# Performance work log

Hardware: AMD Instinct MI355X
Metric: run time of the kernel (lower is better)

Reference implementation:

```python
import jax, jax.numpy as jnp
import numpy as np

NUM_HEADS = 16
HIDDEN = 1024
DIM = HIDDEN // NUM_HEADS  # 64
NEG = -1e8
LN_EPS = 1e-5


def setup_inputs() -> dict:
    key = jax.random.key(0)
    ks = jax.random.split(key, 8)
    B, Lq, Lk = 8, 512, 2048
    s = 0.02
    return {
        "input_embed": jax.random.normal(ks[0], (B, Lq, HIDDEN), jnp.float32),
        "kg_embed": jax.random.normal(ks[1], (B, Lk, HIDDEN), jnp.float32),
        "input_mask": jnp.ones((B, Lq), jnp.float32),
        "kg_mask": jnp.ones((B, Lk), jnp.float32),
        "Wq": jax.random.normal(ks[2], (DIM, DIM), jnp.float32) * s,
        "Wk": jax.random.normal(ks[3], (DIM, DIM), jnp.float32) * s,
        "Wv": jax.random.normal(ks[4], (DIM, DIM), jnp.float32) * s,
        "W_lin": jax.random.normal(ks[5], (HIDDEN, HIDDEN), jnp.float32) * s,
        "b_lin": jnp.zeros((HIDDEN,), jnp.float32),
        "ln_gamma": jnp.ones((HIDDEN,), jnp.float32),
        "ln_beta": jnp.zeros((HIDDEN,), jnp.float32),
    }


def reference(input_embed, kg_embed, input_mask, kg_mask, Wq, Wk, Wv, W_lin, b_lin, ln_gamma, ln_beta):
    B, Lq, H = input_embed.shape
    Lk = kg_embed.shape[1]
    # split heads: per-head slices share the SAME dim x dim q/k/v weights
    xq = input_embed.reshape(B, Lq, NUM_HEADS, DIM)
    xk = kg_embed.reshape(B, Lk, NUM_HEADS, DIM)
    q = jnp.einsum('bqhd,ed->bqhe', xq, Wq)  # Linear: x @ W.T
    k = jnp.einsum('bkhd,ed->bkhe', xk, Wk)
    v = jnp.einsum('bkhd,ed->bkhe', xk, Wv)
    scores = jnp.einsum('bqhd,bkhd->bhqk', q, k) / np.sqrt(DIM)  # [B,H,Lq,Lk]
    # additive masks: query-side and key-side
    scores = scores + ((1.0 - input_mask) * NEG)[:, None, :, None] \
                    + ((1.0 - kg_mask) * NEG)[:, None, None, :]
    attn = jax.nn.softmax(scores, axis=-1)
    ctx = jnp.einsum('bhqk,bkhd->bqhd', attn, v).reshape(B, Lq, H)  # concat heads
    lin = ctx @ W_lin.T + b_lin
    x = jax.nn.gelu(lin, approximate=False) + input_embed  # nn.GELU() is exact erf
    mu = jnp.mean(x, axis=-1, keepdims=True)
    var = jnp.mean(jnp.square(x - mu), axis=-1, keepdims=True)
    return (x - mu) * jax.lax.rsqrt(var + LN_EPS) * ln_gamma + ln_beta
```

## Files before the change

### kernel.cpp

```cpp
#include <hip/hip_runtime.h>
#include <cstdint>

#define BATCH 8
#define LQ 512
#define LK 2048
#define NH 16
#define DIM 64
#define HID 1024
#define NTOK (BATCH * LQ)
#define NKT (LK / 64)
#define SC 0.1803368801111204f
#define NEGM (-1.4426950408889634e8f)

typedef _Float16 f16x8 __attribute__((ext_vector_type(8)));
typedef __fp16 half2v __attribute__((ext_vector_type(2)));
typedef float f32x4 __attribute__((ext_vector_type(4)));

#define MFMA(a, b, c) __builtin_amdgcn_mfma_f32_16x16x32_f16((a), (b), (c), 0, 0, 0)

__device__ __forceinline__ f16x8 ld8(const _Float16* p) { return *(const f16x8*)p; }

__device__ __forceinline__ void gl_lds16(const void* g, void* l) {
  __builtin_amdgcn_global_load_lds(
      (const __attribute__((address_space(1))) uint32_t*)g,
      (__attribute__((address_space(3))) uint32_t*)l, 16, 0, 0);
}

__device__ __forceinline__ f16x8 cvt8(const float* p) {
  const float4 a = *(const float4*)p;
  const float4 b = *(const float4*)(p + 4);
  f16x8 v;
  v[0] = (_Float16)a.x; v[1] = (_Float16)a.y; v[2] = (_Float16)a.z; v[3] = (_Float16)a.w;
  v[4] = (_Float16)b.x; v[5] = (_Float16)b.y; v[6] = (_Float16)b.z; v[7] = (_Float16)b.w;
  return v;
}

__device__ __forceinline__ uint2 pk4(float a, float b, float c, float d) {
  union { half2v h2[2]; uint2 u; } t;
  t.h2[0] = __builtin_amdgcn_cvt_pkrtz(a, b);
  t.h2[1] = __builtin_amdgcn_cvt_pkrtz(c, d);
  return t.u;
}

__device__ __forceinline__ f16x8 pk8(float4 a, float4 b) {
  union { half2v h2[4]; f16x8 v; } t;
  t.h2[0] = __builtin_amdgcn_cvt_pkrtz(a.x, a.y);
  t.h2[1] = __builtin_amdgcn_cvt_pkrtz(a.z, a.w);
  t.h2[2] = __builtin_amdgcn_cvt_pkrtz(b.x, b.y);
  t.h2[3] = __builtin_amdgcn_cvt_pkrtz(b.z, b.w);
  return t.v;
}

__global__ __launch_bounds__(256, 2) void attn_kernel(
    const float* __restrict__ Xq, const float* __restrict__ Xk,
    const float* __restrict__ Wq, const float* __restrict__ Wk,
    const float* __restrict__ Wv, const float* __restrict__ kg_mask,
    _Float16* __restrict__ ctx) {
  __shared__ __align__(16) float    Xl[2][64 * 64];
  __shared__ __align__(16) _Float16 Kl[64 * 72];
  __shared__ __align__(16) _Float16 Vl[64 * 72];
  __shared__ __align__(16) _Float16 Pl[4][16 * 72];
  const int tid = threadIdx.x;
  const int wave = tid >> 6, lane = tid & 63, l16 = lane & 15, quad = lane >> 4;
  const int b = blockIdx.x >> 4, h = blockIdx.x & 15;
  const int qbase = blockIdx.y * 128;
  const float* Xg = Xk + (size_t)b * LK * HID + h * 64;
  const float* mg = kg_mask + (size_t)b * LK;

  auto stageX = [&](int kt, int nbuf) {
#pragma unroll
    for (int i = 0; i < 4; ++i) {
      const int row = i * 16 + wave * 4 + (lane >> 4);
      const int c = (lane & 15) ^ (row & 7);
      gl_lds16(Xg + (size_t)(kt + row) * HID + c * 4,
               &Xl[nbuf][(i * 16 + wave * 4) * 64]);
    }
  };
  stageX(0, 0);

  f16x8 aq0[2], aq1[2];
  {
    f16x8 wq0[4], wq1[4];
#pragma unroll
    for (int nt = 0; nt < 4; ++nt) {
      const float* wp = Wq + (nt * 16 + l16) * DIM + quad * 8;
      wq0[nt] = cvt8(wp);
      wq1[nt] = cvt8(wp + 32);
    }
#pragma unroll
    for (int qt = 0; qt < 2; ++qt) {
      const int qg = qbase + qt * 64 + wave * 16 + l16;
      const float* xpq = Xq + (size_t)(b * LQ + qg) * HID + h * 64 + quad * 8;
      const f16x8 bq0 = cvt8(xpq), bq1 = cvt8(xpq + 32);
#pragma unroll
      for (int nt = 0; nt < 4; ++nt) {
        f32x4 d = {0.f, 0.f, 0.f, 0.f};
        d = MFMA(wq0[nt], bq0, d);
        d = MFMA(wq1[nt], bq1, d);
        *(uint2*)&Pl[wave][l16 * 72 + nt * 16 + quad * 4] =
            pk4(d[0] * SC, d[1] * SC, d[2] * SC, d[3] * SC);
      }
      aq0[qt] = ld8(&Pl[wave][l16 * 72 + quad * 8]);
      aq1[qt] = ld8(&Pl[wave][l16 * 72 + 32 + quad * 8]);
    }
  }

  f16x8 ak0[4], ak1[4], bv0[4], bv1[4];
#pragma unroll
  for (int nt = 0; nt < 4; ++nt) {
    const float* wp = Wk + (nt * 16 + l16) * DIM + quad * 8;
    ak0[nt] = cvt8(wp);
    ak1[nt] = cvt8(wp + 32);
    const float* vp = Wv + (nt * 16 + l16) * DIM + quad * 8;
    bv0[nt] = cvt8(vp);
    bv1[nt] = cvt8(vp + 32);
  }

  const f32x4 z4 = {0.f, 0.f, 0.f, 0.f};
  f32x4 o[2][4];
  float l_run[2] = {0.f, 0.f};
#pragma unroll
  for (int qt = 0; qt < 2; ++qt)
#pragma unroll
    for (int i = 0; i < 4; ++i) o[qt][i] = z4;

  for (int t = 0; t < NKT; ++t) {
    const int buf = t & 1;
    const int kt = t * 64;
    __syncthreads();

    const int rr = wave * 16 + l16;
    const float* xrow = &Xl[buf][rr * 64];
    const int sw8 = l16 & 7;
    const float4 c0 = *(const float4*)(xrow + (((2 * quad) ^ sw8) * 4));
    const float4 c1 = *(const float4*)(xrow + (((2 * quad + 1) ^ sw8) * 4));
    const float4 c2 = *(const float4*)(xrow + (((2 * quad + 8) ^ sw8) * 4));
    const float4 c3 = *(const float4*)(xrow + (((2 * quad + 9) ^ sw8) * 4));
    const f16x8 bx0 = pk8(c0, c1), bx1 = pk8(c2, c3);

#pragma unroll
    for (int nt = 0; nt < 4; ++nt) {
      f32x4 d = z4;
      d = MFMA(ak0[nt], bx0, d);
      d = MFMA(ak1[nt], bx1, d);
      *(uint2*)&Kl[(wave * 16 + l16) * 72 + nt * 16 + quad * 4] =
          pk4(d[0], d[1], d[2], d[3]);
    }
#pragma unroll
    for (int dt = 0; dt < 4; ++dt) {
      f32x4 d = z4;
      d = MFMA(bx0, bv0[dt], d);
      d = MFMA(bx1, bv1[dt], d);
      *(uint2*)&Vl[(dt * 16 + l16) * 72 + wave * 16 + quad * 4] =
          pk4(d[0], d[1], d[2], d[3]);
    }
    __syncthreads();

    float4 mv[4];
#pragma unroll
    for (int nt = 0; nt < 4; ++nt) {
      const float4 m4 = *(const float4*)(mg + kt + nt * 16 + quad * 4);
      mv[nt].x = (1.f - m4.x) * NEGM;
      mv[nt].y = (1.f - m4.y) * NEGM;
      mv[nt].z = (1.f - m4.z) * NEGM;
      mv[nt].w = (1.f - m4.w) * NEGM;
    }
    if (t + 1 < NKT) stageX(kt + 64, buf ^ 1);

    float p[2][4][4];
#pragma unroll
    for (int nt = 0; nt < 4; ++nt) {
      const f16x8 kb0 = ld8(&Kl[(nt * 16 + l16) * 72 + quad * 8]);
      const f16x8 kb1 = ld8(&Kl[(nt * 16 + l16) * 72 + 32 + quad * 8]);
#pragma unroll
      for (int qt = 0; qt < 2; ++qt) {
        f32x4 s = z4;
        s = MFMA(kb0, aq0[qt], s);
        s = MFMA(kb1, aq1[qt], s);
        const float e0 = __builtin_amdgcn_exp2f(s[0] + mv[nt].x);
        const float e1 = __builtin_amdgcn_exp2f(s[1] + mv[nt].y);
        const float e2 = __builtin_amdgcn_exp2f(s[2] + mv[nt].z);
        const float e3 = __builtin_amdgcn_exp2f(s[3] + mv[nt].w);
        l_run[qt] += (e0 + e1) + (e2 + e3);
        p[qt][nt][0] = e0; p[qt][nt][1] = e1; p[qt][nt][2] = e2; p[qt][nt][3] = e3;
      }
    }
    f16x8 ap0[2], ap1[2];
#pragma unroll
    for (int qt = 0; qt < 2; ++qt) {
#pragma unroll
      for (int nt = 0; nt < 4; ++nt)
        *(uint2*)&Pl[wave][l16 * 72 + nt * 16 + quad * 4] =
            pk4(p[qt][nt][0], p[qt][nt][1], p[qt][nt][2], p[qt][nt][3]);
      ap0[qt] = ld8(&Pl[wave][l16 * 72 + quad * 8]);
      ap1[qt] = ld8(&Pl[wave][l16 * 72 + 32 + quad * 8]);
    }
#pragma unroll
    for (int dt = 0; dt < 4; ++dt) {
      const f16x8 vb0 = ld8(&Vl[(dt * 16 + l16) * 72 + quad * 8]);
      const f16x8 vb1 = ld8(&Vl[(dt * 16 + l16) * 72 + 32 + quad * 8]);
#pragma unroll
      for (int qt = 0; qt < 2; ++qt) {
        o[qt][dt] = MFMA(vb0, ap0[qt], o[qt][dt]);
        o[qt][dt] = MFMA(vb1, ap1[qt], o[qt][dt]);
      }
    }
  }

  float inv[2];
#pragma unroll
  for (int qt = 0; qt < 2; ++qt) {
    float s = l_run[qt];
    s += __shfl_xor(s, 16);
    s += __shfl_xor(s, 32);
    inv[qt] = 1.f / s;
  }
#pragma unroll
  for (int qt = 0; qt < 2; ++qt) {
    const int qg = qbase + qt * 64 + wave * 16 + l16;
    _Float16* base = ctx + (size_t)(b * LQ + qg) * HID + h * 64;
#pragma unroll
    for (int dt = 0; dt < 4; ++dt)
      *(uint2*)(base + dt * 16 + quad * 4) =
          pk4(o[qt][dt][0] * inv[qt], o[qt][dt][1] * inv[qt],
              o[qt][dt][2] * inv[qt], o[qt][dt][3] * inv[qt]);
  }
}

__global__ __launch_bounds__(256) void wconv_kernel(const float* __restrict__ W,
                                                    _Float16* __restrict__ Wh) {
  const int i = blockIdx.x * 256 + threadIdx.x;
  const float4 v = ((const float4*)W)[i];
  ((uint2*)Wh)[i] = pk4(v.x, v.y, v.z, v.w);
}

__global__ __launch_bounds__(512) void linear_kernel(const _Float16* __restrict__ A,
                                                     const _Float16* __restrict__ Wh,
                                                     const float* __restrict__ bias,
                                                     const float* __restrict__ resid,
                                                     float* __restrict__ Xout) {
  __shared__ __align__(16) _Float16 Al[2][128 * 64];
  __shared__ __align__(16) _Float16 Bl[2][128 * 64];
  const int tid = threadIdx.x;
  const int wave = tid >> 6, lane = tid & 63, l16 = lane & 15, quad = lane >> 4;
  const int wm = wave >> 2, wn = wave & 3;
  const int nbase = blockIdx.x * 128, mbase = blockIdx.y * 128;
  const int srow = wave * 16 + (lane >> 3);
  const int sc = lane & 7;

  auto stage = [&](int kk, int nbuf) {
#pragma unroll
    for (int i = 0; i < 2; ++i) {
      const int row = srow + i * 8;
      const int c = sc ^ (row & 7);
      gl_lds16(A + (size_t)(mbase + row) * HID + kk + c * 8,
               &Al[nbuf][(wave * 16 + i * 8) * 64]);
      gl_lds16(Wh + (size_t)(nbase + row) * HID + kk + c * 8,
               &Bl[nbuf][(wave * 16 + i * 8) * 64]);
    }
  };

  const f32x4 z4 = {0.f, 0.f, 0.f, 0.f};
  f32x4 acc[4][2];
#pragma unroll
  for (int mt = 0; mt < 4; ++mt)
#pragma unroll
    for (int nt = 0; nt < 2; ++nt) acc[mt][nt] = z4;

  stage(0, 0);
  for (int t = 0; t < HID / 64; ++t) {
    const int buf = t & 1;
    __syncthreads();
    if (t + 1 < HID / 64) stage((t + 1) * 64, buf ^ 1);
    const int sw = l16 & 7;
    f16x8 b0[2], b1[2];
#pragma unroll
    for (int nt = 0; nt < 2; ++nt) {
      const int brow = wn * 32 + nt * 16 + l16;
      b0[nt] = ld8(&Bl[buf][brow * 64 + (quad ^ sw) * 8]);
      b1[nt] = ld8(&Bl[buf][brow * 64 + ((quad + 4) ^ sw) * 8]);
    }
#pragma unroll
    for (int mt = 0; mt < 4; ++mt) {
      const int arow = wm * 64 + mt * 16 + l16;
      const f16x8 a0 = ld8(&Al[buf][arow * 64 + (quad ^ sw) * 8]);
      const f16x8 a1 = ld8(&Al[buf][arow * 64 + ((quad + 4) ^ sw) * 8]);
#pragma unroll
      for (int nt = 0; nt < 2; ++nt) {
        acc[mt][nt] = MFMA(a0, b0[nt], acc[mt][nt]);
        acc[mt][nt] = MFMA(a1, b1[nt], acc[mt][nt]);
      }
    }
  }
#pragma unroll
  for (int nt = 0; nt < 2; ++nt) {
    const int col = nbase + wn * 32 + nt * 16 + l16;
    const float bv = bias[col];
#pragma unroll
    for (int mt = 0; mt < 4; ++mt) {
#pragma unroll
      for (int r = 0; r < 4; ++r) {
        const int row = mbase + wm * 64 + mt * 16 + quad * 4 + r;
        const float v = acc[mt][nt][r] + bv;
        const float g = 0.5f * v * (1.f + erff(v * 0.70710678118654752f));
        Xout[(size_t)row * HID + col] = g + resid[(size_t)row * HID + col];
      }
    }
  }
}

__global__ __launch_bounds__(256) void ln_kernel(const float* __restrict__ X,
                                                 const float* __restrict__ gamma,
                                                 const float* __restrict__ beta,
                                                 float* __restrict__ out) {
  const int row = blockIdx.x, tid = threadIdx.x;
  const int lane = tid & 63, wave = tid >> 6;
  const float4 v = *(const float4*)(X + (size_t)row * HID + tid * 4);
  float s1 = v.x + v.y + v.z + v.w;
  float s2 = v.x * v.x + v.y * v.y + v.z * v.z + v.w * v.w;
#pragma unroll
  for (int off = 1; off < 64; off <<= 1) {
    s1 += __shfl_xor(s1, off);
    s2 += __shfl_xor(s2, off);
  }
  __shared__ float r1[4], r2[4];
  if (lane == 0) { r1[wave] = s1; r2[wave] = s2; }
  __syncthreads();
  s1 = r1[0] + r1[1] + r1[2] + r1[3];
  s2 = r2[0] + r2[1] + r2[2] + r2[3];
  const float mu = s1 * (1.f / HID);
  const float var = s2 * (1.f / HID) - mu * mu;
  const float rstd = rsqrtf(var + 1e-5f);
  const float4 g = *(const float4*)(gamma + tid * 4);
  const float4 be = *(const float4*)(beta + tid * 4);
  float4 ov;
  ov.x = (v.x - mu) * rstd * g.x + be.x;
  ov.y = (v.y - mu) * rstd * g.y + be.y;
  ov.z = (v.z - mu) * rstd * g.z + be.z;
  ov.w = (v.w - mu) * rstd * g.w + be.w;
  *(float4*)(out + (size_t)row * HID + tid * 4) = ov;
}

extern "C" void kernel_launch(void* const* d_in, const int* in_sizes, int n_in,
                              void* d_out, int out_size, void* d_ws, size_t ws_size,
                              hipStream_t stream) {
  (void)in_sizes; (void)n_in; (void)out_size; (void)ws_size;
  const float* input_embed = (const float*)d_in[0];
  const float* kg_embed    = (const float*)d_in[1];
  const float* kg_mask = (const float*)d_in[3];
  const float* Wq    = (const float*)d_in[4];
  const float* Wk    = (const float*)d_in[5];
  const float* Wv    = (const float*)d_in[6];
  const float* W_lin = (const float*)d_in[7];
  const float* b_lin = (const float*)d_in[8];
  const float* gamma = (const float*)d_in[9];
  const float* beta  = (const float*)d_in[10];

  char* ws = (char*)d_ws;
  _Float16* ctx = (_Float16*)(ws);
  float*    Xb  = (float*)(ws + (8u << 20));
  _Float16* Wh  = (_Float16*)(ws + (24u << 20));

  attn_kernel<<<dim3(128, 4), dim3(256), 0, stream>>>(input_embed, kg_embed, Wq, Wk, Wv,
                                                      kg_mask, ctx);
  wconv_kernel<<<dim3(1024), dim3(256), 0, stream>>>(W_lin, Wh);
  linear_kernel<<<dim3(8, 32), dim3(512), 0, stream>>>(ctx, Wh, b_lin, input_embed, Xb);
  ln_kernel<<<dim3(NTOK), dim3(256), 0, stream>>>(Xb, gamma, beta, (float*)d_out);
}
```

Before: 226.9 us.

## Prefetch K/V source rows into registers and double-buffer projected K/V in LDS

The fp32 LDS staging buffer for kg_embed and its async global-to-LDS copies are removed. Each lane now loads its X row slice directly into registers one tile ahead, while projected K and V go into double-buffered LDS. This drops one __syncthreads per iteration and cuts LDS use, which allows three blocks per CU in the launch bounds. The risks are more register pressure under the tighter bound and a row padding of 68 halves (136 bytes), which may not keep 16-byte alignment for the f16x8 LDS loads.

```diff
diff --git a/kernel.cpp b/kernel.cpp
--- a/kernel.cpp
+++ b/kernel.cpp
@@ -9,6 +9,7 @@
 #define HID 1024
 #define NTOK (BATCH * LQ)
 #define NKT (LK / 64)
+#define STR 68
 #define SC 0.1803368801111204f
 #define NEGM (-1.4426950408889634e8f)
 
@@ -51,32 +52,25 @@
   return t.v;
 }
 
-__global__ __launch_bounds__(256, 2) void attn_kernel(
+__global__ __launch_bounds__(256, 3) void attn_kernel(
     const float* __restrict__ Xq, const float* __restrict__ Xk,
     const float* __restrict__ Wq, const float* __restrict__ Wk,
     const float* __restrict__ Wv, const float* __restrict__ kg_mask,
     _Float16* __restrict__ ctx) {
-  __shared__ __align__(16) float    Xl[2][64 * 64];
-  __shared__ __align__(16) _Float16 Kl[64 * 72];
-  __shared__ __align__(16) _Float16 Vl[64 * 72];
-  __shared__ __align__(16) _Float16 Pl[4][16 * 72];
+  __shared__ __align__(16) _Float16 Kl[2][64 * STR];
+  __shared__ __align__(16) _Float16 Vl[2][64 * STR];
+  __shared__ __align__(16) _Float16 Pl[4][16 * STR];
   const int tid = threadIdx.x;
   const int wave = tid >> 6, lane = tid & 63, l16 = lane & 15, quad = lane >> 4;
   const int b = blockIdx.x >> 4, h = blockIdx.x & 15;
   const int qbase = blockIdx.y * 128;
-  const float* Xg = Xk + (size_t)b * LK * HID + h * 64;
   const float* mg = kg_mask + (size_t)b * LK;
-
-  auto stageX = [&](int kt, int nbuf) {
-#pragma unroll
-    for (int i = 0; i < 4; ++i) {
-      const int row = i * 16 + wave * 4 + (lane >> 4);
-      const int c = (lane & 15) ^ (row & 7);
-      gl_lds16(Xg + (size_t)(kt + row) * HID + c * 4,
-               &Xl[nbuf][(i * 16 + wave * 4) * 64]);
-    }
-  };
-  stageX(0, 0);
+  const float* xr0 = Xk + (size_t)(b * LK + wave * 16 + l16) * HID + h * 64 + quad * 8;
+
+  float4 xa = *(const float4*)(xr0);
+  float4 xb = *(const float4*)(xr0 + 4);
+  float4 xc = *(const float4*)(xr0 + 32);
+  float4 xd = *(const float4*)(xr0 + 36);
 
   f16x8 aq0[2], aq1[2];
   {
@@ -97,11 +91,11 @@
         f32x4 d = {0.f, 0.f, 0.f, 0.f};
         d = MFMA(wq0[nt], bq0, d);
         d = MFMA(wq1[nt], bq1, d);
-        *(uint2*)&Pl[wave][l16 * 72 + nt * 16 + quad * 4] =
+        *(uint2*)&Pl[wave][l16 * STR + nt * 16 + quad * 4] =
             pk4(d[0] * SC, d[1] * SC, d[2] * SC, d[3] * SC);
       }
-      aq0[qt] = ld8(&Pl[wave][l16 * 72 + quad * 8]);
-      aq1[qt] = ld8(&Pl[wave][l16 * 72 + 32 + quad * 8]);
+      aq0[qt] = ld8(&Pl[wave][l16 * STR + quad * 8]);
+      aq1[qt] = ld8(&Pl[wave][l16 * STR + 32 + quad * 8]);
     }
   }
 
@@ -127,35 +121,15 @@
   for (int t = 0; t < NKT; ++t) {
     const int buf = t & 1;
     const int kt = t * 64;
-    __syncthreads();
-
-    const int rr = wave * 16 + l16;
-    const float* xrow = &Xl[buf][rr * 64];
-    const int sw8 = l16 & 7;
-    const float4 c0 = *(const float4*)(xrow + (((2 * quad) ^ sw8) * 4));
-    const float4 c1 = *(const float4*)(xrow + (((2 * quad + 1) ^ sw8) * 4));
-    const float4 c2 = *(const float4*)(xrow + (((2 * quad + 8) ^ sw8) * 4));
-    const float4 c3 = *(const float4*)(xrow + (((2 * quad + 9) ^ sw8) * 4));
-    const f16x8 bx0 = pk8(c0, c1), bx1 = pk8(c2, c3);
-
-#pragma unroll
-    for (int nt = 0; nt < 4; ++nt) {
-      f32x4 d = z4;
-      d = MFMA(ak0[nt], bx0, d);
-      d = MFMA(ak1[nt], bx1, d);
-      *(uint2*)&Kl[(wave * 16 + l16) * 72 + nt * 16 + quad * 4] =
-          pk4(d[0], d[1], d[2], d[3]);
-    }
-#pragma unroll
-    for (int dt = 0; dt < 4; ++dt) {
-      f32x4 d = z4;
-      d = MFMA(bx0, bv0[dt], d);
-      d = MFMA(bx1, bv1[dt], d);
-      *(uint2*)&Vl[(dt * 16 + l16) * 72 + wave * 16 + quad * 4] =
-          pk4(d[0], d[1], d[2], d[3]);
-    }
-    __syncthreads();
-
+
+    const f16x8 bx0 = pk8(xa, xb), bx1 = pk8(xc, xd);
+    if (t + 1 < NKT) {
+      const float* xr = xr0 + (size_t)(kt + 64) * HID;
+      xa = *(const float4*)(xr);
+      xb = *(const float4*)(xr + 4);
+      xc = *(const float4*)(xr + 32);
+      xd = *(const float4*)(xr + 36);
+    }
     float4 mv[4];
 #pragma unroll
     for (int nt = 0; nt < 4; ++nt) {
@@ -165,13 +139,30 @@
       mv[nt].z = (1.f - m4.z) * NEGM;
       mv[nt].w = (1.f - m4.w) * NEGM;
     }
-    if (t + 1 < NKT) stageX(kt + 64, buf ^ 1);
+
+#pragma unroll
+    for (int nt = 0; nt < 4; ++nt) {
+      f32x4 d = z4;
+      d = MFMA(ak0[nt], bx0, d);
+      d = MFMA(ak1[nt], bx1, d);
+      *(uint2*)&Kl[buf][(wave * 16 + l16) * STR + nt * 16 + quad * 4] =
+          pk4(d[0], d[1], d[2], d[3]);
+    }
+#pragma unroll
+    for (int dt = 0; dt < 4; ++dt) {
+      f32x4 d = z4;
+      d = MFMA(bx0, bv0[dt], d);
+      d = MFMA(bx1, bv1[dt], d);
+      *(uint2*)&Vl[buf][(dt * 16 + l16) * STR + wave * 16 + quad * 4] =
+          pk4(d[0], d[1], d[2], d[3]);
+    }
+    __syncthreads();
 
     float p[2][4][4];
 #pragma unroll
     for (int nt = 0; nt < 4; ++nt) {
-      const f16x8 kb0 = ld8(&Kl[(nt * 16 + l16) * 72 + quad * 8]);
-      const f16x8 kb1 = ld8(&Kl[(nt * 16 + l16) * 72 + 32 + quad * 8]);
+      const f16x8 kb0 = ld8(&Kl[buf][(nt * 16 + l16) * STR + quad * 8]);
+      const f16x8 kb1 = ld8(&Kl[buf][(nt * 16 + l16) * STR + 32 + quad * 8]);
 #pragma unroll
       for (int qt = 0; qt < 2; ++qt) {
         f32x4 s = z4;
@@ -190,15 +181,15 @@
     for (int qt = 0; qt < 2; ++qt) {
 #pragma unroll
       for (int nt = 0; nt < 4; ++nt)
-        *(uint2*)&Pl[wave][l16 * 72 + nt * 16 + quad * 4] =
+        *(uint2*)&Pl[wave][l16 * STR + nt * 16 + quad * 4] =
             pk4(p[qt][nt][0], p[qt][nt][1], p[qt][nt][2], p[qt][nt][3]);
-      ap0[qt] = ld8(&Pl[wave][l16 * 72 + quad * 8]);
-      ap1[qt] = ld8(&Pl[wave][l16 * 72 + 32 + quad * 8]);
+      ap0[qt] = ld8(&Pl[wave][l16 * STR + quad * 8]);
+      ap1[qt] = ld8(&Pl[wave][l16 * STR + 32 + quad * 8]);
     }
 #pragma unroll
     for (int dt = 0; dt < 4; ++dt) {
-      const f16x8 vb0 = ld8(&Vl[(dt * 16 + l16) * 72 + quad * 8]);
-      const f16x8 vb1 = ld8(&Vl[(dt * 16 + l16) * 72 + 32 + quad * 8]);
+      const f16x8 vb0 = ld8(&Vl[buf][(dt * 16 + l16) * STR + quad * 8]);
+      const f16x8 vb1 = ld8(&Vl[buf][(dt * 16 + l16) * STR + 32 + quad * 8]);
 #pragma unroll
       for (int qt = 0; qt < 2; ++qt) {
         o[qt][dt] = MFMA(vb0, ap0[qt], o[qt][dt]);
```

After: 390.9 us. 72.3% more time.
